# Performance work log

Measured on AMD Instinct MI355X. Metric: run time of the kernel, lower is better.

Reference implementation:

```python
import jax, jax.numpy as jnp
import numpy as np
import math

S, B, D, H, NL, K = 64, 1024, 512, 8, 4, 32
DH = D // H
DFF = 4 * D


def _pe():
    # sinusoidal positional encoding, shape [S, 1, D], scaled by 1/sqrt(D)
    pos = np.arange(S, dtype=np.float32)[:, None]
    div = np.exp(np.arange(0, D, 2, dtype=np.float32) * (-math.log(10000.0) / D))
    pe = np.zeros((S, D), dtype=np.float32)
    pe[:, 0::2] = np.sin(pos * div)
    pe[:, 1::2] = np.cos(pos * div)
    return jnp.asarray(pe[:, None, :] / math.sqrt(D))


def _ln(x, g, b, eps=1e-5):
    m = jnp.mean(x, axis=-1, keepdims=True)
    v = jnp.mean(jnp.square(x - m), axis=-1, keepdims=True)
    return (x - m) * jax.lax.rsqrt(v + eps) * g + b


def setup_inputs() -> dict:
    key = jax.random.key(0)
    ks = jax.random.split(key, 16)
    s = 0.02
    return {
        "x": jax.random.normal(ks[0], (S, B, D), dtype=jnp.float32),
        "ln1_g": jnp.ones((NL, D), jnp.float32),
        "ln1_b": jnp.zeros((NL, D), jnp.float32),
        "qkv_w": jax.random.normal(ks[1], (NL, 3 * D, D), jnp.float32) * s,
        "qkv_b": jnp.zeros((NL, 3 * D), jnp.float32),
        "out_w": jax.random.normal(ks[2], (NL, D, D), jnp.float32) * s,
        "out_b": jnp.zeros((NL, D), jnp.float32),
        "ln2_g": jnp.ones((NL, D), jnp.float32),
        "ln2_b": jnp.zeros((NL, D), jnp.float32),
        "mlp_w1": jax.random.normal(ks[3], (NL, DFF, D), jnp.float32) * s,
        "mlp_b1": jnp.zeros((NL, DFF), jnp.float32),
        "mlp_w2": jax.random.normal(ks[4], (NL, D, DFF), jnp.float32) * s,
        "mlp_b2": jnp.zeros((NL, D), jnp.float32),
        "hash_w": jax.random.normal(ks[5], (K, D), jnp.float32) * s,
        "hash_b": jnp.zeros((K,), jnp.float32),
    }


def reference(x, ln1_g, ln1_b, qkv_w, qkv_b, out_w, out_b,
              ln2_g, ln2_b, mlp_w1, mlp_b1, mlp_w2, mlp_b2,
              hash_w, hash_b):
    # positional encoding (dropout p=0.0 is identity)
    x = x + _pe()
    scale = 1.0 / math.sqrt(DH)
    for i in range(NL):
        # pre-LN multi-head self-attention
        h = _ln(x, ln1_g[i], ln1_b[i])
        qkv = h @ qkv_w[i].T + qkv_b[i]                      # [S,B,3D]
        q, k, v = jnp.split(qkv, 3, axis=-1)
        q = q.reshape(S, B, H, DH)
        k = k.reshape(S, B, H, DH)
        v = v.reshape(S, B, H, DH)
        scores = jnp.einsum('sbhd,tbhd->bhst', q, k) * scale  # [B,H,S,S]
        attn = jax.nn.softmax(scores, axis=-1)
        o = jnp.einsum('bhst,tbhd->sbhd', attn, v).reshape(S, B, D)
        x = x + o @ out_w[i].T + out_b[i]
        # pre-LN MLP with QuickGELU
        h = _ln(x, ln2_g[i], ln2_b[i])
        h1 = h @ mlp_w1[i].T + mlp_b1[i]
        h1 = h1 * jax.nn.sigmoid(1.702 * h1)
        x = x + h1 @ mlp_w2[i].T + mlp_b2[i]
    # BitwiseHashing: per-bit Linear(D,1) applied per seq position, mean over S,
    # concat over k bits, tanh -> equals tanh(mean_S(x) @ W^T + b)
    pooled = jnp.mean(x, axis=0)                              # [B,D]
    return jnp.tanh(pooled @ hash_w.T + hash_b)               # [B,K]
```

## Files before the change

kernel.cpp:

```cpp
#include <hip/hip_runtime.h>
#include <hip/hip_bf16.h>
#include <math.h>

#define S_   64
#define B_   1024
#define D_   512
#define H_   8
#define NL_  4
#define DH_  64
#define DFF_ 2048
#define NTOK (S_*B_)

typedef __bf16 bf16;
typedef __bf16 bf16x8 __attribute__((ext_vector_type(8)));
typedef float  f32x4  __attribute__((ext_vector_type(4)));

#define AS1(p) ((__attribute__((address_space(1))) void*)(void*)(p))
#define AS3(p) ((__attribute__((address_space(3))) void*)(p))

__global__ __launch_bounds__(256) void cvt_k(const float* __restrict__ s,
                                             bf16* __restrict__ d, int n) {
    int i = (blockIdx.x * 256 + threadIdx.x) * 4;
    if (i < n) {
        float4 v = *(const float4*)(s + i);
        bf16 o4[4] = {(bf16)v.x, (bf16)v.y, (bf16)v.z, (bf16)v.w};
        *(ushort4*)(d + i) = *(const ushort4*)o4;
    }
}

__global__ __launch_bounds__(256) void pe_add_k(const float* __restrict__ x,
                                                float* __restrict__ X) {
    int id = blockIdx.x * 256 + threadIdx.x;
    int n = id >> 8;
    int j = id & 255;
    int s = n >> 10;
    float div = expf((float)j * -0.03597789207803197f);
    float ang = (float)s * div;
    const float inv = 0.04419417382415922f;
    float2 v = *(const float2*)(x + (long)n * 512 + 2 * j);
    v.x += sinf(ang) * inv;
    v.y += cosf(ang) * inv;
    *(float2*)(X + (long)n * 512 + 2 * j) = v;
}

__global__ __launch_bounds__(256) void ln_k(const float* __restrict__ X,
                                            const float* __restrict__ g,
                                            const float* __restrict__ be,
                                            bf16* __restrict__ out) {
    long row = (long)blockIdx.x * 4 + (threadIdx.x >> 6);
    int lane = threadIdx.x & 63;
    const float* xr = X + row * 512 + lane * 8;
    float4 v0 = *(const float4*)xr;
    float4 v1 = *(const float4*)(xr + 4);
    float vv[8] = {v0.x, v0.y, v0.z, v0.w, v1.x, v1.y, v1.z, v1.w};
    float s = 0.f, sq = 0.f;
    #pragma unroll
    for (int j = 0; j < 8; j++) { s += vv[j]; sq += vv[j] * vv[j]; }
    #pragma unroll
    for (int off = 1; off < 64; off <<= 1) {
        s  += __shfl_xor(s, off);
        sq += __shfl_xor(sq, off);
    }
    float mean = s * (1.f / 512.f);
    float var  = sq * (1.f / 512.f) - mean * mean;
    float rs = rsqrtf(var + 1e-5f);
    int d = lane * 8;
    bf16 o8[8];
    #pragma unroll
    for (int j = 0; j < 8; j++)
        o8[j] = (bf16)((vv[j] - mean) * rs * g[d + j] + be[d + j]);
    *(uint4*)(out + row * 512 + d) = *(const uint4*)o8;
}

template<int EPI>
__global__ __launch_bounds__(256)
void gemm_bt(const bf16* __restrict__ A, const bf16* __restrict__ Bw,
             const float* __restrict__ bias, float* __restrict__ Xres,
             bf16* __restrict__ Obf, int Mdim, int K) {
    __shared__ bf16 As[128 * 32];
    __shared__ bf16 Bs[128 * 32];
    const int tid  = threadIdx.x;
    const int lane = tid & 63;
    const int wave = tid >> 6;
    const long rowBlk = (long)blockIdx.y * 128;
    const long colBlk = (long)blockIdx.x * 128;

    const int c0 = tid;
    const bf16* ag0 = A  + (rowBlk + (c0 >> 2)) * K + (c0 & 3) * 8;
    const bf16* ag1 = ag0 + 64 * (long)K;
    const bf16* bg0 = Bw + (colBlk + (c0 >> 2)) * K + (c0 & 3) * 8;
    const bf16* bg1 = bg0 + 64 * (long)K;
    bf16* al0 = As + c0 * 8;
    bf16* al1 = As + (c0 + 256) * 8;
    bf16* bl0 = Bs + c0 * 8;
    bf16* bl1 = Bs + (c0 + 256) * 8;

    const int wm = (wave >> 1) * 64, wn = (wave & 1) * 64;
    const int lr = lane & 15, lq = lane >> 4;

    f32x4 acc[4][4] = {};

    for (int k0 = 0; k0 < K; k0 += 32) {
        __builtin_amdgcn_global_load_lds(AS1(ag0 + k0), AS3(al0), 16, 0, 0);
        __builtin_amdgcn_global_load_lds(AS1(ag1 + k0), AS3(al1), 16, 0, 0);
        __builtin_amdgcn_global_load_lds(AS1(bg0 + k0), AS3(bl0), 16, 0, 0);
        __builtin_amdgcn_global_load_lds(AS1(bg1 + k0), AS3(bl1), 16, 0, 0);
        __syncthreads();
        bf16x8 af[4], bfr[4];
        #pragma unroll
        for (int mi = 0; mi < 4; mi++)
            af[mi] = *(const bf16x8*)(As + (wm + mi * 16 + lr) * 32 + lq * 8);
        #pragma unroll
        for (int ni = 0; ni < 4; ni++)
            bfr[ni] = *(const bf16x8*)(Bs + (wn + ni * 16 + lr) * 32 + lq * 8);
        #pragma unroll
        for (int mi = 0; mi < 4; mi++)
            #pragma unroll
            for (int ni = 0; ni < 4; ni++)
                acc[mi][ni] = __builtin_amdgcn_mfma_f32_16x16x32_bf16(
                    af[mi], bfr[ni], acc[mi][ni], 0, 0, 0);
        __syncthreads();
    }

    #pragma unroll
    for (int mi = 0; mi < 4; mi++) {
        #pragma unroll
        for (int ni = 0; ni < 4; ni++) {
            #pragma unroll
            for (int r = 0; r < 4; r++) {
                long row = rowBlk + wm + mi * 16 + lq * 4 + r;
                long col = colBlk + wn + ni * 16 + lr;
                float v = acc[mi][ni][r] + bias[col];
                if (EPI == 0) {
                    Obf[row * Mdim + col] = (bf16)v;
                } else if (EPI == 1) {
                    float gv = v / (1.f + __expf(-1.702f * v));
                    Obf[row * Mdim + col] = (bf16)gv;
                } else {
                    Xres[row * Mdim + col] += v;
                }
            }
        }
    }
}

__global__ __launch_bounds__(256)
void attn_k(const bf16* __restrict__ qkv, bf16* __restrict__ o) {
    __shared__ bf16 qs[64 * 64], ks[64 * 64], vts[64 * 64], ps[64 * 64];
    const int tid = threadIdx.x;
    const int b = blockIdx.x >> 3;
    const int h = blockIdx.x & 7;
    const int lane = tid & 63;
    const int w = tid >> 6;

    #pragma unroll
    for (int half = 0; half < 2; half++) {
        int c = tid + half * 256;
        int trow = c >> 3;
        int off = (c & 7) * 8;
        const bf16* base = qkv + ((long)(trow * B_ + b)) * 1536 + h * 64 + off;
        *(uint4*)(qs + trow * 64 + off) = *(const uint4*)(base);
        *(uint4*)(ks + trow * 64 + off) = *(const uint4*)(base + 512);
        uint4 vv = *(const uint4*)(base + 1024);
        bf16 vtmp[8];
        *(uint4*)vtmp = vv;
        #pragma unroll
        for (int j = 0; j < 8; j++) vts[(off + j) * 64 + trow] = vtmp[j];
    }
    __syncthreads();

    const int lr = lane & 15, lq = lane >> 4;

    f32x4 sc[4] = {};
    #pragma unroll
    for (int d0 = 0; d0 < 64; d0 += 32) {
        bf16x8 aq = *(const bf16x8*)(qs + (w * 16 + lr) * 64 + d0 + lq * 8);
        #pragma unroll
        for (int ni = 0; ni < 4; ni++) {
            bf16x8 bk = *(const bf16x8*)(ks + (ni * 16 + lr) * 64 + d0 + lq * 8);
            sc[ni] = __builtin_amdgcn_mfma_f32_16x16x32_bf16(aq, bk, sc[ni], 0, 0, 0);
        }
    }
    float p[4][4];
    #pragma unroll
    for (int r = 0; r < 4; r++) {
        float m = -1e30f;
        #pragma unroll
        for (int ni = 0; ni < 4; ni++) { sc[ni][r] *= 0.125f; m = fmaxf(m, sc[ni][r]); }
        #pragma unroll
        for (int off = 1; off < 16; off <<= 1) m = fmaxf(m, __shfl_xor(m, off));
        float sum = 0.f;
        #pragma unroll
        for (int ni = 0; ni < 4; ni++) { p[ni][r] = __expf(sc[ni][r] - m); sum += p[ni][r]; }
        #pragma unroll
        for (int off = 1; off < 16; off <<= 1) sum += __shfl_xor(sum, off);
        float inv = 1.f / sum;
        #pragma unroll
        for (int ni = 0; ni < 4; ni++)
            ps[(w * 16 + lq * 4 + r) * 64 + ni * 16 + lr] = (bf16)(p[ni][r] * inv);
    }
    __syncthreads();

    f32x4 oa[4] = {};
    #pragma unroll
    for (int t0 = 0; t0 < 64; t0 += 32) {
        bf16x8 ap = *(const bf16x8*)(ps + (w * 16 + lr) * 64 + t0 + lq * 8);
        #pragma unroll
        for (int ni = 0; ni < 4; ni++) {
            bf16x8 bv = *(const bf16x8*)(vts + (ni * 16 + lr) * 64 + t0 + lq * 8);
            oa[ni] = __builtin_amdgcn_mfma_f32_16x16x32_bf16(ap, bv, oa[ni], 0, 0, 0);
        }
    }
    #pragma unroll
    for (int ni = 0; ni < 4; ni++) {
        #pragma unroll
        for (int r = 0; r < 4; r++) {
            int s = w * 16 + lq * 4 + r;
            int d = ni * 16 + lr;
            o[((long)(s * B_ + b)) * 512 + h * 64 + d] = (bf16)oa[ni][r];
        }
    }
}

__global__ __launch_bounds__(256)
void poolhash_k(const float* __restrict__ X, const float* __restrict__ hw,
                const float* __restrict__ hb, float* __restrict__ out) {
    __shared__ float pooled[512];
    __shared__ float part[8][32];
    int b = blockIdx.x, tid = threadIdx.x;
    for (int d = tid; d < 512; d += 256) {
        float acc = 0.f;
        #pragma unroll 8
        for (int s = 0; s < 64; s++) acc += X[((long)(s * B_ + b)) * 512 + d];
        pooled[d] = acc * (1.f / 64.f);
    }
    __syncthreads();
    int k = tid & 31, ch = tid >> 5;
    float p = 0.f;
    for (int d = ch * 64; d < ch * 64 + 64; d++) p += pooled[d] * hw[k * 512 + d];
    part[ch][k] = p;
    __syncthreads();
    if (tid < 32) {
        float t = hb[tid];
        #pragma unroll
        for (int c = 0; c < 8; c++) t += part[c][tid];
        out[b * 32 + tid] = tanhf(t);
    }
}

extern "C" void kernel_launch(void* const* d_in, const int* in_sizes, int n_in,
                              void* d_out, int out_size, void* d_ws, size_t ws_size,
                              hipStream_t stream) {
    const float* x      = (const float*)d_in[0];
    const float* ln1_g  = (const float*)d_in[1];
    const float* ln1_b  = (const float*)d_in[2];
    const float* qkv_w  = (const float*)d_in[3];
    const float* qkv_b  = (const float*)d_in[4];
    const float* out_w  = (const float*)d_in[5];
    const float* out_b  = (const float*)d_in[6];
    const float* ln2_g  = (const float*)d_in[7];
    const float* ln2_b  = (const float*)d_in[8];
    const float* mlp_w1 = (const float*)d_in[9];
    const float* mlp_b1 = (const float*)d_in[10];
    const float* mlp_w2 = (const float*)d_in[11];
    const float* mlp_b2 = (const float*)d_in[12];
    const float* hash_w = (const float*)d_in[13];
    const float* hash_b = (const float*)d_in[14];

    char* ws = (char*)d_ws;
    float* X  = (float*)ws;
    bf16* BIG = (bf16*)(ws + 134217728);
    bf16* Hb  = (bf16*)(ws + 134217728 + 268435456);
    size_t wo = 134217728 + 268435456 + 67108864;
    bf16* Wq = (bf16*)(ws + wo);            wo += (size_t)NL_ * 1536 * 512 * 2;
    bf16* Wo = (bf16*)(ws + wo);            wo += (size_t)NL_ * 512 * 512 * 2;
    bf16* W1 = (bf16*)(ws + wo);            wo += (size_t)NL_ * 2048 * 512 * 2;
    bf16* W2 = (bf16*)(ws + wo);            wo += (size_t)NL_ * 512 * 2048 * 2;

    cvt_k<<<(NL_ * 1536 * 512) / 1024, 256, 0, stream>>>(qkv_w,  Wq, NL_ * 1536 * 512);
    cvt_k<<<(NL_ * 512  * 512) / 1024, 256, 0, stream>>>(out_w,  Wo, NL_ * 512  * 512);
    cvt_k<<<(NL_ * 2048 * 512) / 1024, 256, 0, stream>>>(mlp_w1, W1, NL_ * 2048 * 512);
    cvt_k<<<(NL_ * 512 * 2048) / 1024, 256, 0, stream>>>(mlp_w2, W2, NL_ * 512 * 2048);

    pe_add_k<<<(NTOK * 256) / 256, 256, 0, stream>>>(x, X);

    for (int i = 0; i < NL_; i++) {
        ln_k<<<NTOK / 4, 256, 0, stream>>>(X, ln1_g + i * 512, ln1_b + i * 512, Hb);
        gemm_bt<0><<<dim3(12, 512), 256, 0, stream>>>(Hb, Wq + (size_t)i * 1536 * 512,
                                                      qkv_b + i * 1536, nullptr, BIG, 1536, 512);
        attn_k<<<B_ * H_, 256, 0, stream>>>(BIG, Hb);
        gemm_bt<2><<<dim3(4, 512), 256, 0, stream>>>(Hb, Wo + (size_t)i * 512 * 512,
                                                     out_b + i * 512, X, nullptr, 512, 512);
        ln_k<<<NTOK / 4, 256, 0, stream>>>(X, ln2_g + i * 512, ln2_b + i * 512, Hb);
        gemm_bt<1><<<dim3(16, 512), 256, 0, stream>>>(Hb, W1 + (size_t)i * 2048 * 512,
                                                      mlp_b1 + i * 2048, nullptr, BIG, 2048, 512);
        gemm_bt<2><<<dim3(4, 512), 256, 0, stream>>>(BIG, W2 + (size_t)i * 512 * 2048,
                                                     mlp_b2 + i * 512, X, nullptr, 512, 2048);
    }

    poolhash_k<<<B_, 256, 0, stream>>>(X, hash_w, hash_b, (float*)d_out);
}
```

Baseline: 4.377 ms.

## Fuse MLP up-projection, QuickGELU and down-projection into one kernel

Replaces the two MLP GEMM launches with a single kernel. For each 64-row block it computes 128-column chunks of the hidden layer, applies bias and QuickGELU into shared memory, and accumulates the down-projection into registers before adding to the residual. This removes the round trip of the large hidden activation through global memory. In exchange the 64-row tile reloads the A rows for each hidden chunk and streams both weight matrices per block with no double buffering. Heavy shared-memory use may also limit occupancy.

```diff
diff --git a/kernel.cpp b/kernel.cpp
--- a/kernel.cpp
+++ b/kernel.cpp
@@ -133,12 +133,134 @@
                 float v = acc[mi][ni][r] + bias[col];
                 if (EPI == 0) {
                     Obf[row * Mdim + col] = (bf16)v;
-                } else if (EPI == 1) {
-                    float gv = v / (1.f + __expf(-1.702f * v));
-                    Obf[row * Mdim + col] = (bf16)gv;
                 } else {
                     Xres[row * Mdim + col] += v;
                 }
+            }
+        }
+    }
+}
+
+__global__ __launch_bounds__(256, 2)
+void fused_mlp(const bf16* __restrict__ A,
+               const bf16* __restrict__ W1,
+               const float* __restrict__ b1,
+               const bf16* __restrict__ W2,
+               const float* __restrict__ b2,
+               float* __restrict__ X) {
+    __shared__ bf16 As[64 * 128];
+    __shared__ bf16 Ws[16384];
+    __shared__ bf16 h1s[64 * 136];
+    const int tid = threadIdx.x;
+    const int lane = tid & 63;
+    const int w = tid >> 6;
+    const int lr = lane & 15, lq = lane >> 4;
+    const long rowBlk = (long)blockIdx.x * 64;
+
+    f32x4 acc2[4][8] = {};
+
+    for (int j = 0; j < 16; j++) {
+        f32x4 acc1[4][2] = {};
+        for (int kk = 0; kk < 4; kk++) {
+            #pragma unroll
+            for (int r = 0; r < 4; r++) {
+                int c = tid + r * 256;
+                int row = c >> 4, ks = c & 15;
+                int ko = ks ^ (row & 7);
+                __builtin_amdgcn_global_load_lds(
+                    AS1(A + (rowBlk + row) * 512 + kk * 128 + ko * 8),
+                    AS3(As + c * 8), 16, 0, 0);
+            }
+            #pragma unroll
+            for (int r = 0; r < 8; r++) {
+                int c = tid + r * 256;
+                int n = c >> 4, ks = c & 15;
+                int ko = ks ^ (n & 7);
+                __builtin_amdgcn_global_load_lds(
+                    AS1(W1 + ((long)j * 128 + n) * 512 + kk * 128 + ko * 8),
+                    AS3(Ws + c * 8), 16, 0, 0);
+            }
+            __syncthreads();
+            #pragma unroll
+            for (int kh = 0; kh < 4; kh++) {
+                bf16x8 af[4], bfx[2];
+                #pragma unroll
+                for (int ri = 0; ri < 4; ri++) {
+                    int row = ri * 16 + lr;
+                    int ks = (kh * 4 + lq) ^ (row & 7);
+                    af[ri] = *(const bf16x8*)(As + row * 128 + ks * 8);
+                }
+                #pragma unroll
+                for (int ci = 0; ci < 2; ci++) {
+                    int n = w * 32 + ci * 16 + lr;
+                    int ks = (kh * 4 + lq) ^ (n & 7);
+                    bfx[ci] = *(const bf16x8*)(Ws + n * 128 + ks * 8);
+                }
+                #pragma unroll
+                for (int ri = 0; ri < 4; ri++)
+                    #pragma unroll
+                    for (int ci = 0; ci < 2; ci++)
+                        acc1[ri][ci] = __builtin_amdgcn_mfma_f32_16x16x32_bf16(
+                            af[ri], bfx[ci], acc1[ri][ci], 0, 0, 0);
+            }
+            __syncthreads();
+        }
+        #pragma unroll
+        for (int ci = 0; ci < 2; ci++) {
+            int col = w * 32 + ci * 16 + lr;
+            float bv = b1[j * 128 + col];
+            #pragma unroll
+            for (int ri = 0; ri < 4; ri++) {
+                #pragma unroll
+                for (int r = 0; r < 4; r++) {
+                    int row = ri * 16 + lq * 4 + r;
+                    float v = acc1[ri][ci][r] + bv;
+                    float g = v / (1.f + __expf(-1.702f * v));
+                    h1s[row * 136 + col] = (bf16)g;
+                }
+            }
+        }
+        __syncthreads();
+        for (int kk2 = 0; kk2 < 4; kk2++) {
+            #pragma unroll
+            for (int r = 0; r < 8; r++) {
+                int c = tid + r * 256;
+                int n = c >> 2, ks = c & 3;
+                int ko = ks ^ ((n >> 1) & 3);
+                __builtin_amdgcn_global_load_lds(
+                    AS1(W2 + (long)n * 2048 + j * 128 + kk2 * 32 + ko * 8),
+                    AS3(Ws + c * 8), 16, 0, 0);
+            }
+            __syncthreads();
+            bf16x8 af2[4], bf2[8];
+            #pragma unroll
+            for (int ri = 0; ri < 4; ri++)
+                af2[ri] = *(const bf16x8*)(h1s + (ri * 16 + lr) * 136 + kk2 * 32 + lq * 8);
+            #pragma unroll
+            for (int ci = 0; ci < 8; ci++) {
+                int n = w * 128 + ci * 16 + lr;
+                int ks = lq ^ ((n >> 1) & 3);
+                bf2[ci] = *(const bf16x8*)(Ws + n * 32 + ks * 8);
+            }
+            #pragma unroll
+            for (int ri = 0; ri < 4; ri++)
+                #pragma unroll
+                for (int ci = 0; ci < 8; ci++)
+                    acc2[ri][ci] = __builtin_amdgcn_mfma_f32_16x16x32_bf16(
+                        af2[ri], bf2[ci], acc2[ri][ci], 0, 0, 0);
+            __syncthreads();
+        }
+    }
+    #pragma unroll
+    for (int ci = 0; ci < 8; ci++) {
+        int col = w * 128 + ci * 16 + lr;
+        float bv = b2[col];
+        #pragma unroll
+        for (int ri = 0; ri < 4; ri++) {
+            #pragma unroll
+            for (int r = 0; r < 4; r++) {
+                long row = rowBlk + ri * 16 + lq * 4 + r;
+                X[row * 512 + col] += acc2[ri][ci][r] + bv;
             }
         }
     }
@@ -292,10 +414,10 @@
         gemm_bt<2><<<dim3(4, 512), 256, 0, stream>>>(Hb, Wo + (size_t)i * 512 * 512,
                                                      out_b + i * 512, X, nullptr, 512, 512);
         ln_k<<<NTOK / 4, 256, 0, stream>>>(X, ln2_g + i * 512, ln2_b + i * 512, Hb);
-        gemm_bt<1><<<dim3(16, 512), 256, 0, stream>>>(Hb, W1 + (size_t)i * 2048 * 512,
-                                                      mlp_b1 + i * 2048, nullptr, BIG, 2048, 512);
-        gemm_bt<2><<<dim3(4, 512), 256, 0, stream>>>(BIG, W2 + (size_t)i * 512 * 2048,
-                                                     mlp_b2 + i * 512, X, nullptr, 512, 2048);
+        fused_mlp<<<NTOK / 64, 256, 0, stream>>>(Hb, W1 + (size_t)i * 2048 * 512,
+                                                 mlp_b1 + i * 2048,
+                                                 W2 + (size_t)i * 512 * 2048,
+                                                 mlp_b2 + i * 512, X);
     }
 
     poolhash_k<<<B_, 256, 0, stream>>>(X, hash_w, hash_b, (float*)d_out);
```

Measured after the change: 3.742 ms. 1.17x faster.
